# Kernel tuning notes

Measured on AMD Instinct MI355X. Metric: run time of the kernel, lower is better.

## Reference

```python
import jax, jax.numpy as jnp
import numpy as np
import itertools

N = 120000    # occupied voxels
S = 64        # grid side
CIN = 32
COUT = 64
K = 27        # 3x3x3 kernel offsets
TAU = 0.1


def _build_nbr():
    # numpy coordinate hashing == MinkowskiEngine kernel map (stride 1)
    rng = np.random.default_rng(0)
    flat = rng.permutation(S ** 3)[:N].astype(np.int64)
    occ = np.full(S ** 3 + 1, N, dtype=np.int32)  # sentinel N = missing
    occ[flat] = np.arange(N, dtype=np.int32)
    coords = np.stack([flat // (S * S), (flat // S) % S, flat % S], 1)  # (N,3)
    offs = np.array(list(itertools.product([-1, 0, 1], repeat=3)), dtype=np.int64)  # (27,3)
    nb = coords[:, None, :] + offs[None]  # (N,27,3)
    valid = ((nb >= 0) & (nb < S)).all(-1)
    nf = np.where(valid, nb[..., 0] * S * S + nb[..., 1] * S + nb[..., 2], S ** 3)
    return jnp.asarray(np.where(valid, occ[nf], N).astype(np.int32))


def setup_inputs() -> dict:
    key = jax.random.key(0)
    ks = jax.random.split(key, 8)
    x_F = jax.random.normal(ks[0], (N, CIN), jnp.float32)
    W_ch = jax.random.normal(ks[1], (K, CIN, COUT), jnp.float32) * 0.05
    b_ch = jax.random.normal(ks[2], (COUT,), jnp.float32) * 0.05
    W_cls = jax.random.normal(ks[3], (COUT, 2), jnp.float32) * 0.05
    b_cls = jax.random.normal(ks[4], (2,), jnp.float32) * 0.05
    W_dw = jax.random.normal(ks[5], (K, COUT, COUT), jnp.float32) * 0.05
    b_dw = jax.random.normal(ks[6], (COUT,), jnp.float32) * 0.05
    u = jax.random.uniform(ks[7], (N, 2), jnp.float32, 1e-10, 1.0)
    gumbel = -jnp.log(-jnp.log(u))  # fixed gumbel noise (torch.manual_seed(42) analogue)
    return {"x_F": x_F, "gumbel": gumbel, "nbr_idx": _build_nbr(),
            "W_ch": W_ch, "b_ch": b_ch, "W_cls": W_cls, "b_cls": b_cls,
            "W_dw": W_dw, "b_dw": b_dw, "th": 0}


def _sconv(F, W, b, nbr_idx):
    # sparse 3^3 conv, stride 1: gather neighbors (sentinel row = zeros) then per-offset GEMM
    Fp = jnp.concatenate([F, jnp.zeros((1, F.shape[1]), F.dtype)], 0)
    g = Fp[nbr_idx]  # (N, 27, Cin)
    return jnp.einsum('nkc,kcd->nd', g, W) + b


def reference(x_F, gumbel, nbr_idx, W_ch, b_ch, W_cls, b_cls, W_dw, b_dw, th):
    x1 = _sconv(x_F, W_ch, b_ch, nbr_idx)            # Channel_code
    logits = x1 @ W_cls + b_cls                      # 1x1 cls conv
    soft = jax.nn.softmax((logits + gumbel) / TAU, axis=-1)
    hard = jax.nn.one_hot(jnp.argmax(soft, -1), 2, dtype=soft.dtype)
    y = hard + soft - jax.lax.stop_gradient(soft)    # hard gumbel-softmax (straight-through)
    m_s = jax.lax.stop_gradient(hard[:, 0])          # boolean routing masks (no grad, as .bool())
    m_w = jax.lax.stop_gradient(hard[:, 1])
    Fs = x1 * y[:, 0:1] * m_s[:, None]               # strong subset features (weak rows excluded from kernel map)
    Fw = x1 * y[:, 1:2]
    conv_s = _sconv(Fs, W_dw, b_dw, nbr_idx)         # dw conv on strong subset
    out = m_s[:, None] * conv_s + m_w[:, None] * Fw  # union of disjoint coord sets, aligned to x order
    return out + x1
```

## Files before the change

### kernel.cpp

```cpp
#include <hip/hip_runtime.h>

#define NR 120000
#define CI 32
#define CO 64
#define KK 27

#define GLOAD_LDS16(g, l) __builtin_amdgcn_global_load_lds( \
    (const __attribute__((address_space(1))) unsigned int*)(g), \
    (__attribute__((address_space(3))) unsigned int*)(l), 16, 0, 0)

__global__ __launch_bounds__(256, 2)
void k_conv1(const float* __restrict__ xF, const float* __restrict__ gum,
             const int* __restrict__ nbr, const float* __restrict__ Wch,
             const float* __restrict__ bch, const float* __restrict__ Wcls,
             const float* __restrict__ bcls, const float* __restrict__ zbufX,
             float* __restrict__ x1m, int* __restrict__ sids,
             int* __restrict__ cnt, unsigned* __restrict__ mkbits,
             float* __restrict__ outp)
{
    __shared__ float gs[2 * 128 * CI];
    __shared__ float Ws[2][CI * CO];
    __shared__ int   sl[128];
    __shared__ unsigned mwords[4];
    __shared__ int   scnt, sbase;

    const int t    = threadIdx.x;
    const int dq   = t & 15;
    const int rq   = t >> 4;
    const int rq7  = rq & 7;
    const int dq4  = dq * 4;
    const int sr   = t >> 3;
    const int sq   = t & 7;
    const int row0 = blockIdx.x * 128;

    if (t == 0) scnt = 0;
    if (t < 4) mwords[t] = 0u;

    int jr[4];
#pragma unroll
    for (int pp = 0; pp < 4; ++pp) {
        int i = row0 + pp * 32 + sr;
        jr[pp] = (i < NR) ? nbr[i * KK] : NR;
    }
#pragma unroll
    for (int pp = 0; pp < 4; ++pp) {
        int r = pp * 32 + sr;
        const float* gsrc = (jr[pp] < NR) ? (xF + (size_t)jr[pp] * CI)
                                          : (zbufX + (r & 63) * CI);
        GLOAD_LDS16(gsrc + ((sq ^ (r & 7)) << 2), &gs[(pp * 256 + t) * 4]);
    }
    {
        const float4* Wk = (const float4*)Wch;
        float4 a0 = Wk[t], a1 = Wk[t + 256];
        float4* Wv = (float4*)&Ws[0][0];
        Wv[t] = a0; Wv[t + 256] = a1;
    }
#pragma unroll
    for (int pp = 0; pp < 4; ++pp) {
        int i = row0 + pp * 32 + sr;
        jr[pp] = (i < NR) ? nbr[i * KK + 1] : NR;
    }
    float4 wr0, wr1;
    {
        const float4* Wk = (const float4*)(Wch + CI * CO);
        wr0 = Wk[t]; wr1 = Wk[t + 256];
    }

    const float4 bq = ((const float4*)bch)[dq];
    float4 acc[8];
#pragma unroll
    for (int rp = 0; rp < 8; ++rp) acc[rp] = bq;

    float wcA[4], wcB[4];
#pragma unroll
    for (int c = 0; c < 4; ++c) {
        wcA[c] = Wcls[(dq4 + c) * 2];
        wcB[c] = Wcls[(dq4 + c) * 2 + 1];
    }
    const float b0 = bcls[0], b1 = bcls[1];

    int gso = 0, wp = 0;
    __syncthreads();

#pragma unroll 1
    for (int k = 0; k < KK; ++k) {
        if (k < KK - 1) {
#pragma unroll
            for (int pp = 0; pp < 4; ++pp) {
                int r = pp * 32 + sr;
                const float* gsrc = (jr[pp] < NR) ? (xF + (size_t)jr[pp] * CI)
                                                  : (zbufX + (r & 63) * CI);
                GLOAD_LDS16(gsrc + ((sq ^ (r & 7)) << 2),
                            &gs[(gso ^ (128 * CI)) + (pp * 256 + t) * 4]);
            }
            float4* Wv = (float4*)&Ws[wp ^ 1][0];
            Wv[t] = wr0; Wv[t + 256] = wr1;
        }
        if (k < KK - 2) {
#pragma unroll
            for (int pp = 0; pp < 4; ++pp) {
                int i = row0 + pp * 32 + sr;
                jr[pp] = (i < NR) ? nbr[i * KK + k + 2] : NR;
            }
            const float4* Wk = (const float4*)(Wch + (size_t)(k + 2) * CI * CO);
            wr0 = Wk[t]; wr1 = Wk[t + 256];
        }
        const float* gsb = &gs[gso];
        const float* wsb = &Ws[wp][0];
#pragma unroll
        for (int cq = 0; cq < CI / 4; ++cq) {
            float4 w0 = *(const float4*)&wsb[(cq * 4 + 0) * CO + dq4];
            float4 w1 = *(const float4*)&wsb[(cq * 4 + 1) * CO + dq4];
            float4 w2 = *(const float4*)&wsb[(cq * 4 + 2) * CO + dq4];
            float4 w3 = *(const float4*)&wsb[(cq * 4 + 3) * CO + dq4];
            const int cs = ((cq ^ rq7) << 2);
#pragma unroll
            for (int rp = 0; rp < 8; ++rp) {
                float4 g = *(const float4*)&gsb[(rp * 16 + rq) * CI + cs];
                acc[rp].x += g.x * w0.x + g.y * w1.x + g.z * w2.x + g.w * w3.x;
                acc[rp].y += g.x * w0.y + g.y * w1.y + g.z * w2.y + g.w * w3.y;
                acc[rp].z += g.x * w0.z + g.y * w1.z + g.z * w2.z + g.w * w3.z;
                acc[rp].w += g.x * w0.w + g.y * w1.w + g.z * w2.w + g.w * w3.w;
            }
        }
        __syncthreads();
        gso ^= (128 * CI); wp ^= 1;
    }

#pragma unroll
    for (int rp = 0; rp < 8; ++rp) {
        float4 a = acc[rp];
        float p0 = a.x * wcA[0] + a.y * wcA[1] + a.z * wcA[2] + a.w * wcA[3];
        float p1 = a.x * wcB[0] + a.y * wcB[1] + a.z * wcB[2] + a.w * wcB[3];
#pragma unroll
        for (int off = 1; off < 16; off <<= 1) {
            p0 += __shfl_xor(p0, off, 64);
            p1 += __shfl_xor(p1, off, 64);
        }
        int i = row0 + rp * 16 + rq;
        if (i < NR) {
            float z0 = p0 + b0 + gum[2 * i];
            float z1 = p1 + b1 + gum[2 * i + 1];
            bool m = (z0 >= z1);
            ((float4*)(outp + (size_t)i * CO))[dq] =
                make_float4(2.f * a.x, 2.f * a.y, 2.f * a.z, 2.f * a.w);
            float4 xm = m ? a : make_float4(0.f, 0.f, 0.f, 0.f);
            ((float4*)(x1m + (size_t)i * CO))[dq] = xm;
            if (dq == 0 && m) {
                int lr = rp * 16 + rq;
                atomicOr(&mwords[lr >> 5], 1u << (lr & 31));
                int pos = atomicAdd(&scnt, 1); sl[pos] = i;
            }
        }
    }
    __syncthreads();
    if (t < 4) mkbits[(row0 >> 5) + t] = mwords[t];
    if (t == 0) sbase = atomicAdd(cnt, scnt);
    __syncthreads();
    if (t < scnt) sids[sbase + t] = sl[t];
}

__global__ __launch_bounds__(256, 2)
void k_conv2(const float* __restrict__ x1m, const int* __restrict__ nbr,
             const float* __restrict__ Wdw, const float* __restrict__ bdw,
             const int* __restrict__ sids, const int* __restrict__ cnt,
             const unsigned* __restrict__ mkbits, const float* __restrict__ zbuf1,
             float* __restrict__ outp)
{
    const int nstrong = *cnt;
    const int row0 = blockIdx.x * 64;
    if (row0 >= nstrong) return;

    __shared__ float gs[2][64 * CO];
    __shared__ float Ws[2][CO * CO];

    const int t   = threadIdx.x;
    const int dq  = t & 15;
    const int rq  = t >> 4;
    const int dq4 = dq * 4;

    int ssid[4];
#pragma unroll
    for (int p = 0; p < 4; ++p) {
        int rr = row0 + p * 16 + rq;
        ssid[p] = (rr < nstrong) ? sids[rr] : -1;
    }

    int jn[4]; unsigned mw[4];
#pragma unroll
    for (int p = 0; p < 4; ++p)
        jn[p] = (ssid[p] >= 0) ? nbr[ssid[p] * KK] : NR;
#pragma unroll
    for (int p = 0; p < 4; ++p) mw[p] = mkbits[jn[p] >> 5];

#pragma unroll
    for (int p = 0; p < 4; ++p) {
        int r = p * 16 + rq;
        bool s = (mw[p] >> (jn[p] & 31)) & 1u;
        const float* gsrc = s ? (x1m + (size_t)jn[p] * CO) : (zbuf1 + r * CO);
        GLOAD_LDS16(gsrc + ((dq ^ rq) << 2), &gs[0][(p * 256 + t) * 4]);
    }
    float4 w0r, w1r, w2r, w3r;
    {
        const float4* Wk = (const float4*)Wdw;
        w0r = Wk[t]; w1r = Wk[t + 256]; w2r = Wk[t + 512]; w3r = Wk[t + 768];
        float4* Wv = (float4*)&Ws[0][0];
        Wv[t] = w0r; Wv[t + 256] = w1r; Wv[t + 512] = w2r; Wv[t + 768] = w3r;
    }
#pragma unroll
    for (int p = 0; p < 4; ++p)
        jn[p] = (ssid[p] >= 0) ? nbr[ssid[p] * KK + 1] : NR;
#pragma unroll
    for (int p = 0; p < 4; ++p) mw[p] = mkbits[jn[p] >> 5];
    {
        const float4* Wk = (const float4*)(Wdw + (size_t)CO * CO);
        w0r = Wk[t]; w1r = Wk[t + 256]; w2r = Wk[t + 512]; w3r = Wk[t + 768];
    }

    float4 acc[4];
#pragma unroll
    for (int rp = 0; rp < 4; ++rp) acc[rp] = make_float4(0.f, 0.f, 0.f, 0.f);

    int gso = 0, wp = 0;
    __syncthreads();

#pragma unroll 1
    for (int k = 0; k < KK; ++k) {
        if (k < KK - 1) {
#pragma unroll
            for (int p = 0; p < 4; ++p) {
                int r = p * 16 + rq;
                bool s = (mw[p] >> (jn[p] & 31)) & 1u;
                const float* gsrc = s ? (x1m + (size_t)jn[p] * CO)
                                      : (zbuf1 + r * CO);
                GLOAD_LDS16(gsrc + ((dq ^ rq) << 2),
                            &gs[gso ^ 1][(p * 256 + t) * 4]);
            }
            float4* Wv = (float4*)&Ws[wp ^ 1][0];
            Wv[t] = w0r; Wv[t + 256] = w1r; Wv[t + 512] = w2r; Wv[t + 768] = w3r;
        }
        if (k < KK - 2) {
#pragma unroll
            for (int p = 0; p < 4; ++p)
                jn[p] = (ssid[p] >= 0) ? nbr[ssid[p] * KK + k + 2] : NR;
#pragma unroll
            for (int p = 0; p < 4; ++p) mw[p] = mkbits[jn[p] >> 5];
            const float4* Wk = (const float4*)(Wdw + (size_t)(k + 2) * CO * CO);
            w0r = Wk[t]; w1r = Wk[t + 256]; w2r = Wk[t + 512]; w3r = Wk[t + 768];
        }
        const float* gsb = &gs[gso][0];
        const float* wsb = &Ws[wp][0];
#pragma unroll
        for (int cq = 0; cq < CO / 4; ++cq) {
            float4 w0 = *(const float4*)&wsb[(cq * 4 + 0) * CO + dq4];
            float4 w1 = *(const float4*)&wsb[(cq * 4 + 1) * CO + dq4];
            float4 w2 = *(const float4*)&wsb[(cq * 4 + 2) * CO + dq4];
            float4 w3 = *(const float4*)&wsb[(cq * 4 + 3) * CO + dq4];
            const int cs = ((cq ^ rq) & 15) << 2;
#pragma unroll
            for (int rp = 0; rp < 4; ++rp) {
                float4 g = *(const float4*)&gsb[(rp * 16 + rq) * CO + cs];
                acc[rp].x += g.x * w0.x + g.y * w1.x + g.z * w2.x + g.w * w3.x;
                acc[rp].y += g.x * w0.y + g.y * w1.y + g.z * w2.y + g.w * w3.y;
                acc[rp].z += g.x * w0.z + g.y * w1.z + g.z * w2.z + g.w * w3.z;
                acc[rp].w += g.x * w0.w + g.y * w1.w + g.z * w2.w + g.w * w3.w;
            }
        }
        __syncthreads();
        gso ^= 1; wp ^= 1;
    }

    const float4 bq = ((const float4*)bdw)[dq];
#pragma unroll
    for (int rp = 0; rp < 4; ++rp) {
        int rr = row0 + rp * 16 + rq;
        if (rr < nstrong) {
            int sid = ssid[rp];
            float4 xv = ((const float4*)(x1m + (size_t)sid * CO))[dq];
            float4 a = acc[rp];
            ((float4*)(outp + (size_t)sid * CO))[dq] =
                make_float4(a.x + bq.x + xv.x, a.y + bq.y + xv.y,
                            a.z + bq.z + xv.z, a.w + bq.w + xv.w);
        }
    }
}

extern "C" void kernel_launch(void* const* d_in, const int* in_sizes, int n_in,
                              void* d_out, int out_size, void* d_ws, size_t ws_size,
                              hipStream_t stream)
{
    const float* xF   = (const float*)d_in[0];
    const float* gum  = (const float*)d_in[1];
    const int*   nbr  = (const int*)d_in[2];
    const float* Wch  = (const float*)d_in[3];
    const float* bch  = (const float*)d_in[4];
    const float* Wcls = (const float*)d_in[5];
    const float* bcls = (const float*)d_in[6];
    const float* Wdw  = (const float*)d_in[7];
    const float* bdw  = (const float*)d_in[8];

    float* outp = (float*)d_out;
    char*  ws   = (char*)d_ws;

    float*    x1m    = (float*)(ws);
    float*    zbufX  = (float*)(ws + 30720000);
    float*    zbuf1  = (float*)(ws + 30728192);
    int*      cnt    = (int*)(ws + 30744576);
    unsigned* mkbits = (unsigned*)(ws + 30744704);
    int*      sids   = (int*)(ws + 30759744);

    hipMemsetAsync(ws + 30720000, 0, 30759744 - 30720000, stream);

    hipLaunchKernelGGL(k_conv1, dim3((NR + 127) / 128), dim3(256), 0, stream,
                       xF, gum, nbr, Wch, bch, Wcls, bcls, zbufX,
                       x1m, sids, cnt, mkbits, outp);
    hipLaunchKernelGGL(k_conv2, dim3((NR + 63) / 64), dim3(256), 0, stream,
                       x1m, nbr, Wdw, bdw, sids, cnt, mkbits, zbuf1, outp);
}
```

Before: 772.1 us.

## Read conv weights directly from global/L1 instead of staging through LDS

Both sparse-conv kernels stop double-buffering the per-offset weight slice in shared memory. Each thread now loads its weight float4s straight from global memory, software-pipelined one channel group ahead. This removes the LDS weight traffic and staging stores and reduces shared memory use, which allows launch bounds to rise from 2 to 4 blocks per CU. The cost is more global/L1 load traffic and latency inside the inner loop, along with a tighter register budget.

```diff
diff --git a/kernel.cpp b/kernel.cpp
--- a/kernel.cpp
+++ b/kernel.cpp
@@ -9,7 +9,13 @@
     (const __attribute__((address_space(1))) unsigned int*)(g), \
     (__attribute__((address_space(3))) unsigned int*)(l), 16, 0, 0)
 
-__global__ __launch_bounds__(256, 2)
+#define FMA4(acc, g, w0, w1, w2, w3) \
+    acc.x += g.x * w0.x + g.y * w1.x + g.z * w2.x + g.w * w3.x; \
+    acc.y += g.x * w0.y + g.y * w1.y + g.z * w2.y + g.w * w3.y; \
+    acc.z += g.x * w0.z + g.y * w1.z + g.z * w2.z + g.w * w3.z; \
+    acc.w += g.x * w0.w + g.y * w1.w + g.z * w2.w + g.w * w3.w;
+
+__global__ __launch_bounds__(256, 4)
 void k_conv1(const float* __restrict__ xF, const float* __restrict__ gum,
              const int* __restrict__ nbr, const float* __restrict__ Wch,
              const float* __restrict__ bch, const float* __restrict__ Wcls,
@@ -19,7 +25,6 @@
              float* __restrict__ outp)
 {
     __shared__ float gs[2 * 128 * CI];
-    __shared__ float Ws[2][CI * CO];
     __shared__ int   sl[128];
     __shared__ unsigned mwords[4];
     __shared__ int   scnt, sbase;
@@ -49,22 +54,11 @@
                                           : (zbufX + (r & 63) * CI);
         GLOAD_LDS16(gsrc + ((sq ^ (r & 7)) << 2), &gs[(pp * 256 + t) * 4]);
     }
-    {
-        const float4* Wk = (const float4*)Wch;
-        float4 a0 = Wk[t], a1 = Wk[t + 256];
-        float4* Wv = (float4*)&Ws[0][0];
-        Wv[t] = a0; Wv[t + 256] = a1;
-    }
 #pragma unroll
     for (int pp = 0; pp < 4; ++pp) {
         int i = row0 + pp * 32 + sr;
         jr[pp] = (i < NR) ? nbr[i * KK + 1] : NR;
     }
-    float4 wr0, wr1;
-    {
-        const float4* Wk = (const float4*)(Wch + CI * CO);
-        wr0 = Wk[t]; wr1 = Wk[t + 256];
-    }
 
     const float4 bq = ((const float4*)bch)[dq];
     float4 acc[8];
@@ -79,7 +73,7 @@
     }
     const float b0 = bcls[0], b1 = bcls[1];
 
-    int gso = 0, wp = 0;
+    int gso = 0;
     __syncthreads();
 
 #pragma unroll 1
@@ -93,8 +87,6 @@
                 GLOAD_LDS16(gsrc + ((sq ^ (r & 7)) << 2),
                             &gs[(gso ^ (128 * CI)) + (pp * 256 + t) * 4]);
             }
-            float4* Wv = (float4*)&Ws[wp ^ 1][0];
-            Wv[t] = wr0; Wv[t + 256] = wr1;
         }
         if (k < KK - 2) {
 #pragma unroll
@@ -102,29 +94,44 @@
                 int i = row0 + pp * 32 + sr;
                 jr[pp] = (i < NR) ? nbr[i * KK + k + 2] : NR;
             }
-            const float4* Wk = (const float4*)(Wch + (size_t)(k + 2) * CI * CO);
-            wr0 = Wk[t]; wr1 = Wk[t + 256];
         }
         const float* gsb = &gs[gso];
-        const float* wsb = &Ws[wp][0];
-#pragma unroll
-        for (int cq = 0; cq < CI / 4; ++cq) {
-            float4 w0 = *(const float4*)&wsb[(cq * 4 + 0) * CO + dq4];
-            float4 w1 = *(const float4*)&wsb[(cq * 4 + 1) * CO + dq4];
-            float4 w2 = *(const float4*)&wsb[(cq * 4 + 2) * CO + dq4];
-            float4 w3 = *(const float4*)&wsb[(cq * 4 + 3) * CO + dq4];
-            const int cs = ((cq ^ rq7) << 2);
-#pragma unroll
-            for (int rp = 0; rp < 8; ++rp) {
-                float4 g = *(const float4*)&gsb[(rp * 16 + rq) * CI + cs];
-                acc[rp].x += g.x * w0.x + g.y * w1.x + g.z * w2.x + g.w * w3.x;
-                acc[rp].y += g.x * w0.y + g.y * w1.y + g.z * w2.y + g.w * w3.y;
-                acc[rp].z += g.x * w0.z + g.y * w1.z + g.z * w2.z + g.w * w3.z;
-                acc[rp].w += g.x * w0.w + g.y * w1.w + g.z * w2.w + g.w * w3.w;
+        const float* Wg  = Wch + (size_t)k * CI * CO;
+        float4 wa0 = *(const float4*)(Wg + 0 * CO + dq4);
+        float4 wa1 = *(const float4*)(Wg + 1 * CO + dq4);
+        float4 wa2 = *(const float4*)(Wg + 2 * CO + dq4);
+        float4 wa3 = *(const float4*)(Wg + 3 * CO + dq4);
+#pragma unroll
+        for (int cq = 0; cq < 8; cq += 2) {
+            float4 wb0 = *(const float4*)(Wg + ((cq + 1) * 4 + 0) * CO + dq4);
+            float4 wb1 = *(const float4*)(Wg + ((cq + 1) * 4 + 1) * CO + dq4);
+            float4 wb2 = *(const float4*)(Wg + ((cq + 1) * 4 + 2) * CO + dq4);
+            float4 wb3 = *(const float4*)(Wg + ((cq + 1) * 4 + 3) * CO + dq4);
+            {
+                const int cs = ((cq ^ rq7) << 2);
+#pragma unroll
+                for (int rp = 0; rp < 8; ++rp) {
+                    float4 g = *(const float4*)&gsb[(rp * 16 + rq) * CI + cs];
+                    FMA4(acc[rp], g, wa0, wa1, wa2, wa3)
+                }
+            }
+            if (cq + 2 < 8) {
+                wa0 = *(const float4*)(Wg + ((cq + 2) * 4 + 0) * CO + dq4);
+                wa1 = *(const float4*)(Wg + ((cq + 2) * 4 + 1) * CO + dq4);
+                wa2 = *(const float4*)(Wg + ((cq + 2) * 4 + 2) * CO + dq4);
+                wa3 = *(const float4*)(Wg + ((cq + 2) * 4 + 3) * CO + dq4);
+            }
+            {
+                const int cs = (((cq + 1) ^ rq7) << 2);
+#pragma unroll
+                for (int rp = 0; rp < 8; ++rp) {
+                    float4 g = *(const float4*)&gsb[(rp * 16 + rq) * CI + cs];
+                    FMA4(acc[rp], g, wb0, wb1, wb2, wb3)
+                }
             }
         }
         __syncthreads();
-        gso ^= (128 * CI); wp ^= 1;
+        gso ^= (128 * CI);
     }
 
 #pragma unroll
@@ -160,7 +167,7 @@
     if (t < scnt) sids[sbase + t] = sl[t];
 }
 
-__global__ __launch_bounds__(256, 2)
+__global__ __launch_bounds__(256, 4)
 void k_conv2(const float* __restrict__ x1m, const int* __restrict__ nbr,
              const float* __restrict__ Wdw, const float* __restrict__ bdw,
              const int* __restrict__ sids, const int* __restrict__ cnt,
@@ -172,7 +179,6 @@
     if (row0 >= nstrong) return;
 
     __shared__ float gs[2][64 * CO];
-    __shared__ float Ws[2][CO * CO];
 
     const int t   = threadIdx.x;
     const int dq  = t & 15;
@@ -192,7 +198,6 @@
         jn[p] = (ssid[p] >= 0) ? nbr[ssid[p] * KK] : NR;
 #pragma unroll
     for (int p = 0; p < 4; ++p) mw[p] = mkbits[jn[p] >> 5];
-
 #pragma unroll
     for (int p = 0; p < 4; ++p) {
         int r = p * 16 + rq;
@@ -200,28 +205,17 @@
         const float* gsrc = s ? (x1m + (size_t)jn[p] * CO) : (zbuf1 + r * CO);
         GLOAD_LDS16(gsrc + ((dq ^ rq) << 2), &gs[0][(p * 256 + t) * 4]);
     }
-    float4 w0r, w1r, w2r, w3r;
-    {
-        const float4* Wk = (const float4*)Wdw;
-        w0r = Wk[t]; w1r = Wk[t + 256]; w2r = Wk[t + 512]; w3r = Wk[t + 768];
-        float4* Wv = (float4*)&Ws[0][0];
-        Wv[t] = w0r; Wv[t + 256] = w1r; Wv[t + 512] = w2r; Wv[t + 768] = w3r;
-    }
 #pragma unroll
     for (int p = 0; p < 4; ++p)
         jn[p] = (ssid[p] >= 0) ? nbr[ssid[p] * KK + 1] : NR;
 #pragma unroll
     for (int p = 0; p < 4; ++p) mw[p] = mkbits[jn[p] >> 5];
-    {
-        const float4* Wk = (const float4*)(Wdw + (size_t)CO * CO);
-        w0r = Wk[t]; w1r = Wk[t + 256]; w2r = Wk[t + 512]; w3r = Wk[t + 768];
-    }
 
     float4 acc[4];
 #pragma unroll
     for (int rp = 0; rp < 4; ++rp) acc[rp] = make_float4(0.f, 0.f, 0.f, 0.f);
 
-    int gso = 0, wp = 0;
+    int gso = 0;
     __syncthreads();
 
 #pragma unroll 1
@@ -236,8 +230,6 @@
                 GLOAD_LDS16(gsrc + ((dq ^ rq) << 2),
                             &gs[gso ^ 1][(p * 256 + t) * 4]);
             }
-            float4* Wv = (float4*)&Ws[wp ^ 1][0];
-            Wv[t] = w0r; Wv[t + 256] = w1r; Wv[t + 512] = w2r; Wv[t + 768] = w3r;
         }
         if (k < KK - 2) {
 #pragma unroll
@@ -245,29 +237,44 @@
                 jn[p] = (ssid[p] >= 0) ? nbr[ssid[p] * KK + k + 2] : NR;
 #pragma unroll
             for (int p = 0; p < 4; ++p) mw[p] = mkbits[jn[p] >> 5];
-            const float4* Wk = (const float4*)(Wdw + (size_t)(k + 2) * CO * CO);
-            w0r = Wk[t]; w1r = Wk[t + 256]; w2r = Wk[t + 512]; w3r = Wk[t + 768];
         }
         const float* gsb = &gs[gso][0];
-        const float* wsb = &Ws[wp][0];
-#pragma unroll
-        for (int cq = 0; cq < CO / 4; ++cq) {
-            float4 w0 = *(const float4*)&wsb[(cq * 4 + 0) * CO + dq4];
-            float4 w1 = *(const float4*)&wsb[(cq * 4 + 1) * CO + dq4];
-            float4 w2 = *(const float4*)&wsb[(cq * 4 + 2) * CO + dq4];
-            float4 w3 = *(const float4*)&wsb[(cq * 4 + 3) * CO + dq4];
-            const int cs = ((cq ^ rq) & 15) << 2;
-#pragma unroll
-            for (int rp = 0; rp < 4; ++rp) {
-                float4 g = *(const float4*)&gsb[(rp * 16 + rq) * CO + cs];
-                acc[rp].x += g.x * w0.x + g.y * w1.x + g.z * w2.x + g.w * w3.x;
-                acc[rp].y += g.x * w0.y + g.y * w1.y + g.z * w2.y + g.w * w3.y;
-                acc[rp].z += g.x * w0.z + g.y * w1.z + g.z * w2.z + g.w * w3.z;
-                acc[rp].w += g.x * w0.w + g.y * w1.w + g.z * w2.w + g.w * w3.w;
+        const float* Wg  = Wdw + (size_t)k * CO * CO;
+        float4 wa0 = *(const float4*)(Wg + 0 * CO + dq4);
+        float4 wa1 = *(const float4*)(Wg + 1 * CO + dq4);
+        float4 wa2 = *(const float4*)(Wg + 2 * CO + dq4);
+        float4 wa3 = *(const float4*)(Wg + 3 * CO + dq4);
+#pragma unroll
+        for (int cq = 0; cq < 16; cq += 2) {
+            float4 wb0 = *(const float4*)(Wg + ((cq + 1) * 4 + 0) * CO + dq4);
+            float4 wb1 = *(const float4*)(Wg + ((cq + 1) * 4 + 1) * CO + dq4);
+            float4 wb2 = *(const float4*)(Wg + ((cq + 1) * 4 + 2) * CO + dq4);
+            float4 wb3 = *(const float4*)(Wg + ((cq + 1) * 4 + 3) * CO + dq4);
+            {
+                const int cs = ((cq ^ rq) & 15) << 2;
+#pragma unroll
+                for (int rp = 0; rp < 4; ++rp) {
+                    float4 g = *(const float4*)&gsb[(rp * 16 + rq) * CO + cs];
+                    FMA4(acc[rp], g, wa0, wa1, wa2, wa3)
+                }
+            }
+            if (cq + 2 < 16) {
+                wa0 = *(const float4*)(Wg + ((cq + 2) * 4 + 0) * CO + dq4);
+                wa1 = *(const float4*)(Wg + ((cq + 2) * 4 + 1) * CO + dq4);
+                wa2 = *(const float4*)(Wg + ((cq + 2) * 4 + 2) * CO + dq4);
+                wa3 = *(const float4*)(Wg + ((cq + 2) * 4 + 3) * CO + dq4);
+            }
+            {
+                const int cs = (((cq + 1) ^ rq) & 15) << 2;
+#pragma unroll
+                for (int rp = 0; rp < 4; ++rp) {
+                    float4 g = *(const float4*)&gsb[(rp * 16 + rq) * CO + cs];
+                    FMA4(acc[rp], g, wb0, wb1, wb2, wb3)
+                }
             }
         }
         __syncthreads();
-        gso ^= 1; wp ^= 1;
+        gso ^= 1;
     }
 
     const float4 bq = ((const float4*)bdw)[dq];
```

Result: slower. 2.884 ms (+273.5%).
